# Performance work log

Hardware: AMD Instinct MI355X
Metric: run time of the kernel (lower is better)

Reference implementation:

```python
import jax, jax.numpy as jnp
import numpy as np
import math

N, D, F = 8192, 512, 2048
M, K = 4096, 128  # masked cells, masked genes per cell
EPS = 1e-5


def setup_inputs() -> dict:
    key = jax.random.key(0)
    ks = jax.random.split(key, 16)
    s = 0.02
    x = jax.random.normal(ks[0], (N, D), jnp.float32)
    # distinct masked cell indices (torch.randperm semantics)
    mask_nodes = jax.random.permutation(ks[1], N)[:M].astype(jnp.int64)
    # per-row distinct gene indices (torch.randperm per row)
    gene_idx = jnp.argsort(jax.random.uniform(ks[2], (M, D)), axis=1)[:, :K].astype(jnp.int64)
    return {
        'x': x, 'mask_nodes': mask_nodes, 'gene_idx': gene_idx,
        'Wq_e': s * jax.random.normal(ks[3], (D, D), jnp.float32),
        'Wk_e': s * jax.random.normal(ks[4], (D, D), jnp.float32),
        'Wv_e': s * jax.random.normal(ks[5], (D, D), jnp.float32),
        'ln1_g': jnp.ones((D,), jnp.float32), 'ln1_b': jnp.zeros((D,), jnp.float32),
        'ff_W1': s * jax.random.normal(ks[6], (D, F), jnp.float32),
        'ff_b1': jnp.zeros((F,), jnp.float32),
        'ff_W2': s * jax.random.normal(ks[7], (F, D), jnp.float32),
        'ff_b2': jnp.zeros((D,), jnp.float32),
        'ln2_g': jnp.ones((D,), jnp.float32), 'ln2_b': jnp.zeros((D,), jnp.float32),
        'Wq_d': s * jax.random.normal(ks[8], (D, D), jnp.float32),
        'Wk_d': s * jax.random.normal(ks[9], (D, D), jnp.float32),
        'Wv_d': s * jax.random.normal(ks[10], (D, D), jnp.float32),
        'ln3_g': jnp.ones((D,), jnp.float32), 'ln3_b': jnp.zeros((D,), jnp.float32),
        'ln4_g': jnp.ones((D,), jnp.float32), 'ln4_b': jnp.zeros((D,), jnp.float32),
        'head_W': s * jax.random.normal(ks[11], (D, D), jnp.float32),
        'head_b': jnp.zeros((D,), jnp.float32),
    }


def _ln(h, g, b):
    mu = jnp.mean(h, axis=-1, keepdims=True)
    var = jnp.mean(jnp.square(h - mu), axis=-1, keepdims=True)
    return (h - mu) * jax.lax.rsqrt(var + EPS) * g + b


def _attn(h, Wq, Wk, Wv):
    Q = h @ Wq
    Kt = h @ Wk
    V = h @ Wv
    scores = (Q @ Kt.T) / math.sqrt(D)  # [N, N]
    attn = jax.nn.softmax(scores, axis=-1)
    return attn @ V, attn


def _ff(h, W1, b1, W2, b2):
    return jax.nn.gelu(h @ W1 + b1, approximate=False) @ W2 + b2


def reference(x, mask_nodes, gene_idx,
              Wq_e, Wk_e, Wv_e, ln1_g, ln1_b,
              ff_W1, ff_b1, ff_W2, ff_b2, ln2_g, ln2_b,
              Wq_d, Wk_d, Wv_d, ln3_g, ln3_b, ln4_g, ln4_b,
              head_W, head_b):
    # mask selected genes of selected cells to 0 (encoding_mask_nodes)
    rows = mask_nodes[:, None]
    use_x = x.at[rows, gene_idx].set(0.0)

    hidden, encode_weights = _attn(use_x, Wq_e, Wk_e, Wv_e)
    hidden = _ln(hidden + use_x, ln1_g, ln1_b)
    hidden = _ln(hidden + _ff(hidden, ff_W1, ff_b1, ff_W2, ff_b2), ln2_g, ln2_b)
    # NOTE: `hidden[mask_nodes][gene_mask] = 0` in the original torch code
    # writes into a copy produced by advanced indexing -> it is a no-op.

    recon, _ = _attn(hidden, Wq_d, Wk_d, Wv_d)
    recon = _ln(recon + hidden, ln3_g, ln3_b)
    # original reuses self.ff (not self.ff1) in the decoder block
    recon = _ln(recon + _ff(recon, ff_W1, ff_b1, ff_W2, ff_b2), ln4_g, ln4_b)
    h = recon @ head_W + head_b

    x_init = x[rows, gene_idx]      # [M, K]
    x_recon = h[rows, gene_idx]     # [M, K]
    return (x_init, x_recon, encode_weights, recon)
```

## Files before the change

kernel.cpp:

```cpp
#include <hip/hip_runtime.h>
#include <hip/hip_bf16.h>
#include <stdint.h>
#include <math.h>

typedef __bf16 bf16_t;
typedef __bf16 bf16x8 __attribute__((ext_vector_type(8)));
typedef __bf16 bf16x4 __attribute__((ext_vector_type(4)));
typedef float floatx4 __attribute__((ext_vector_type(4)));

#define NN 8192
#define DD 512
#define FF 2048
#define MM 4096
#define KK 128

template<typename T> struct V16;
template<> struct V16<bf16_t> { using t = bf16x8;  static const int sh = 3; };
template<> struct V16<float>  { using t = floatx4; static const int sh = 2; };

__device__ __forceinline__ void async_copy16(const void* g, void* l) {
    __builtin_amdgcn_global_load_lds(
        (const __attribute__((address_space(1))) void*)(uintptr_t)g,
        (__attribute__((address_space(3))) void*)(uint32_t)(uintptr_t)l,
        16, 0, 0);
}

template<int EPI, typename OT>
__global__ __launch_bounds__(256)
void gemm_nt(const bf16_t* __restrict__ A, const bf16_t* __restrict__ B,
             OT* __restrict__ C,
             int M, int Nc, int Kd, int ldA, int ldB, int ldC,
             long partStride, float scale, const float* __restrict__ bias,
             float* __restrict__ denom)
{
    __shared__ char smem[16384];
    bf16_t* As = (bf16_t*)smem;
    bf16_t* Bs = (bf16_t*)(smem + 8192);

    const int tid  = threadIdx.x;
    const int lane = tid & 63;
    const int wave = tid >> 6;
    const int wm   = (wave >> 1) << 6;
    const int wn   = (wave & 1) << 6;
    const int quad = lane >> 4;
    const int l16  = lane & 15;

    const int gx   = gridDim.x;
    const int nwg  = gx * gridDim.y;
    const int orig = blockIdx.y * gx + blockIdx.x;
    const int swz  = (orig & 7) * (nwg >> 3) + (orig >> 3);
    const long bm  = (long)(swz % gx) * 128;
    const long bn  = (long)(swz / gx) * 128;

    const int  kchunk = Kd / gridDim.z;
    const long kBeg   = (long)blockIdx.z * kchunk;
    OT* __restrict__ Co = C + (long)blockIdx.z * partStride;

    const int t0 = tid, t1 = tid + 256;
    const bf16_t* pA0 = A + (bm + (t0 >> 2)) * (long)ldA + (t0 & 3) * 8 + kBeg;
    const bf16_t* pA1 = A + (bm + (t1 >> 2)) * (long)ldA + (t1 & 3) * 8 + kBeg;
    const bf16_t* pB0 = B + (bn + (t0 >> 2)) * (long)ldB + (t0 & 3) * 8 + kBeg;
    const bf16_t* pB1 = B + (bn + (t1 >> 2)) * (long)ldB + (t1 & 3) * 8 + kBeg;
    bf16_t* lA0 = &As[t0 * 8];
    bf16_t* lA1 = &As[t1 * 8];
    bf16_t* lB0 = &Bs[t0 * 8];
    bf16_t* lB1 = &Bs[t1 * 8];

    floatx4 acc[4][4] = {};

    for (long k0 = 0; k0 < kchunk; k0 += 32) {
        async_copy16(pA0 + k0, lA0);
        async_copy16(pA1 + k0, lA1);
        async_copy16(pB0 + k0, lB0);
        async_copy16(pB1 + k0, lB1);
        __syncthreads();

        bf16x8 af[4], bfr[4];
#pragma unroll
        for (int i = 0; i < 4; i++) {
            af[i]  = *(const bf16x8*)&As[(wm + i * 16 + l16) * 32 + quad * 8];
            bfr[i] = *(const bf16x8*)&Bs[(wn + i * 16 + l16) * 32 + quad * 8];
        }
#pragma unroll
        for (int mi = 0; mi < 4; mi++)
#pragma unroll
            for (int ni = 0; ni < 4; ni++)
                acc[mi][ni] = __builtin_amdgcn_mfma_f32_16x16x32_bf16(
                    af[mi], bfr[ni], acc[mi][ni], 0, 0, 0);
        __syncthreads();
    }

    OT* sm = (OT*)smem;
    const int g = wm >> 6;
#pragma unroll
    for (int mi = 0; mi < 4; mi++) {
        if (mi) __syncthreads();
        const long rbase = bm + wm + mi * 16 + quad * 4;
        if (EPI == 4) {
#pragma unroll
            for (int r = 0; r < 4; r++) {
                float rsum = 0.0f;
#pragma unroll
                for (int ni = 0; ni < 4; ni++) {
                    float v = __expf(acc[mi][ni][r] * scale);
                    rsum += v;
                    sm[(g * 16 + quad * 4 + r) * 128 + wn + ni * 16 + l16] = (OT)v;
                }
                rsum += __shfl_xor(rsum, 1);
                rsum += __shfl_xor(rsum, 2);
                rsum += __shfl_xor(rsum, 4);
                rsum += __shfl_xor(rsum, 8);
                if (l16 == 0) atomicAdd(denom + rbase + r, rsum);
            }
        } else {
#pragma unroll
            for (int ni = 0; ni < 4; ni++) {
                float bv = (EPI >= 2) ? bias[bn + wn + ni * 16 + l16] : 0.0f;
#pragma unroll
                for (int r = 0; r < 4; r++) {
                    float v = acc[mi][ni][r];
                    if (EPI == 1) v *= scale;
                    if (EPI >= 2) v += bv;
                    if (EPI == 3) v = 0.5f * v * (1.0f + erff(v * 0.70710678118f));
                    sm[(g * 16 + quad * 4 + r) * 128 + wn + ni * 16 + l16] = (OT)v;
                }
            }
        }
        __syncthreads();
        typedef typename V16<OT>::t VT;
        const int VSH = V16<OT>::sh;
        const int VEC = 1 << VSH;
        const int NP  = (32 * 128) / (256 * VEC);
#pragma unroll
        for (int p = 0; p < NP; p++) {
            const int vid  = p * 256 + tid;
            const int lrow = vid >> (7 - VSH);
            const int vcol = vid & ((128 >> VSH) - 1);
            const long grow = bm + (lrow >> 4) * 64 + mi * 16 + (lrow & 15);
            *(VT*)&Co[grow * (long)ldC + bn + vcol * VEC] =
                *(const VT*)&sm[lrow * 128 + vcol * VEC];
        }
    }
}

template<int EPI, typename OT>
static void launch_gemm(const bf16_t* A, const bf16_t* B, OT* C,
                        int M, int Nc, int Kd, int lda, int ldb, int ldc,
                        int splitk, long partStride, float scale,
                        const float* bias, float* denom, hipStream_t s)
{
    dim3 g(M / 128, Nc / 128, splitk);
    gemm_nt<EPI, OT><<<g, 256, 0, s>>>(A, B, C, M, Nc, Kd, lda, ldb, ldc,
                                       partStride, scale, bias, denom);
}

__global__ __launch_bounds__(256)
void transpose_f2b(const float* __restrict__ in, bf16_t* __restrict__ out,
                   int R, int C)
{
    __shared__ float tile[32][33];
    const int bx = blockIdx.x * 32;
    const int by = blockIdx.y * 32;
    const int tx = threadIdx.x, ty = threadIdx.y;
#pragma unroll
    for (int i = 0; i < 32; i += 8)
        tile[ty + i][tx] = in[(long)(by + ty + i) * C + bx + tx];
    __syncthreads();
#pragma unroll
    for (int i = 0; i < 32; i += 8)
        out[(long)(bx + ty + i) * R + by + tx] = (bf16_t)tile[tx][ty + i];
}

__global__ __launch_bounds__(256)
void transpose_b2b(const bf16_t* __restrict__ in, bf16_t* __restrict__ out,
                   int R, int C, int ldin)
{
    __shared__ bf16_t tile[32][34];
    const int bx = blockIdx.x * 32;
    const int by = blockIdx.y * 32;
    const int tx = threadIdx.x, ty = threadIdx.y;
#pragma unroll
    for (int i = 0; i < 32; i += 8)
        tile[ty + i][tx] = in[(long)(by + ty + i) * ldin + bx + tx];
    __syncthreads();
#pragma unroll
    for (int i = 0; i < 32; i += 8)
        out[(long)(bx + ty + i) * R + by + tx] = tile[tx][ty + i];
}

__global__ __launch_bounds__(256)
void encw_norm(const bf16_t* __restrict__ P, const float* __restrict__ denom,
               float* __restrict__ out)
{
    const long row = blockIdx.x;
    const float inv = 1.0f / denom[row];
    const bf16_t* p = P + row * (long)NN;
    float* q = out + row * (long)NN;
    const int tid = threadIdx.x;
#pragma unroll
    for (int i = 0; i < 4; i++) {
        const int o = (tid + i * 256) * 8;
        bf16x8 v = *(const bf16x8*)(p + o);
        float4 lo, hi;
        lo.x = (float)v[0] * inv; lo.y = (float)v[1] * inv;
        lo.z = (float)v[2] * inv; lo.w = (float)v[3] * inv;
        hi.x = (float)v[4] * inv; hi.y = (float)v[5] * inv;
        hi.z = (float)v[6] * inv; hi.w = (float)v[7] * inv;
        *(float4*)(q + o)     = lo;
        *(float4*)(q + o + 4) = hi;
    }
}

__global__ __launch_bounds__(256)
void zero_f32(float* __restrict__ p)
{
    p[blockIdx.x * 256 + threadIdx.x] = 0.0f;
}

template<int NP, bool RS, bool CB>
__global__ __launch_bounds__(64)
void add_ln_gen(const float* __restrict__ a, long pstride,
                const float* __restrict__ rs, const float* __restrict__ cb,
                const float* __restrict__ b,
                const float* __restrict__ g, const float* __restrict__ be,
                bf16_t* __restrict__ ob, float* __restrict__ of)
{
    const long row = blockIdx.x;
    const int lane = threadIdx.x;
    const long base = row * DD + lane * 8;
    const float irs = RS ? (1.0f / rs[row]) : 1.0f;
    float v[8], s = 0.0f, s2 = 0.0f;
#pragma unroll
    for (int j = 0; j < 8; j++) {
        float t = 0.0f;
#pragma unroll
        for (int p = 0; p < NP; p++) t += a[base + j + p * pstride];
        t *= irs;
        if (CB) t += cb[lane * 8 + j];
        t += b[base + j];
        v[j] = t;
        s += t; s2 += t * t;
    }
#pragma unroll
    for (int off = 32; off > 0; off >>= 1) {
        s  += __shfl_xor(s,  off);
        s2 += __shfl_xor(s2, off);
    }
    const float mu  = s * (1.0f / DD);
    const float var = s2 * (1.0f / DD) - mu * mu;
    const float inv = rsqrtf(var + 1e-5f);
    bf16x8 o;
#pragma unroll
    for (int j = 0; j < 8; j++) {
        float r = (v[j] - mu) * inv * g[lane * 8 + j] + be[lane * 8 + j];
        o[j] = (bf16_t)r;
        of[base + j] = r;
    }
    *(bf16x8*)(ob + base) = o;
}

__global__ __launch_bounds__(256)
void build_usex(const float* __restrict__ x, bf16_t* __restrict__ ub,
                float* __restrict__ uf)
{
    const long i = ((long)blockIdx.x * 256 + threadIdx.x) * 4;
    const float4 v = *(const float4*)(x + i);
    *(float4*)(uf + i) = v;
    bf16x4 o = { (bf16_t)v.x, (bf16_t)v.y, (bf16_t)v.z, (bf16_t)v.w };
    *(bf16x4*)(ub + i) = o;
}

__global__ __launch_bounds__(256)
void scatter_zero(bf16_t* __restrict__ ub, float* __restrict__ uf,
                  const int* __restrict__ mn, const int* __restrict__ gi)
{
    const int i = blockIdx.x * 256 + threadIdx.x;
    const long idx = (long)mn[i >> 7] * DD + gi[i];
    ub[idx] = (bf16_t)0.0f;
    uf[idx] = 0.0f;
}

__global__ __launch_bounds__(256)
void gather_mk(const float* __restrict__ src, const int* __restrict__ mn,
               const int* __restrict__ gi, float* __restrict__ dst)
{
    const int i = blockIdx.x * 256 + threadIdx.x;
    dst[i] = src[(long)mn[i >> 7] * DD + gi[i]];
}

__global__ __launch_bounds__(256)
void gather_head(const float* __restrict__ p1, long pstride,
                 const float* __restrict__ hb, const int* __restrict__ mn,
                 const int* __restrict__ gi, float* __restrict__ dst)
{
    const int i = blockIdx.x * 256 + threadIdx.x;
    const int col = gi[i];
    const long idx = (long)mn[i >> 7] * DD + col;
    dst[i] = p1[idx] + p1[idx + pstride] + hb[col];
}

extern "C" void kernel_launch(void* const* d_in, const int* in_sizes, int n_in,
                              void* d_out, int out_size, void* d_ws, size_t ws_size,
                              hipStream_t stream)
{
    const float* x      = (const float*)d_in[0];
    const int*   mn     = (const int*)d_in[1];
    const int*   gi     = (const int*)d_in[2];
    const float* Wq_e   = (const float*)d_in[3];
    const float* Wk_e   = (const float*)d_in[4];
    const float* Wv_e   = (const float*)d_in[5];
    const float* ln1_g  = (const float*)d_in[6];
    const float* ln1_b  = (const float*)d_in[7];
    const float* ff_W1  = (const float*)d_in[8];
    const float* ff_b1  = (const float*)d_in[9];
    const float* ff_W2  = (const float*)d_in[10];
    const float* ff_b2  = (const float*)d_in[11];
    const float* ln2_g  = (const float*)d_in[12];
    const float* ln2_b  = (const float*)d_in[13];
    const float* Wq_d   = (const float*)d_in[14];
    const float* Wk_d   = (const float*)d_in[15];
    const float* Wv_d   = (const float*)d_in[16];
    const float* ln3_g  = (const float*)d_in[17];
    const float* ln3_b  = (const float*)d_in[18];
    const float* ln4_g  = (const float*)d_in[19];
    const float* ln4_b  = (const float*)d_in[20];
    const float* head_W = (const float*)d_in[21];
    const float* head_b = (const float*)d_in[22];

    float* outf     = (float*)d_out;
    float* o_xinit  = outf;
    float* o_xrecon = outf + (size_t)MM * KK;
    float* o_encw   = outf + (size_t)2 * MM * KK;
    float* o_recon  = o_encw + (size_t)NN * NN;

    char* ws = (char*)d_ws;
    size_t off = 0;
    auto alloc = [&](size_t bytes) -> void* {
        void* p = ws + off;
        off += (bytes + 255) & ~(size_t)255;
        return p;
    };
    const size_t NDb = (size_t)NN * DD * sizeof(bf16_t);
    const size_t NDf = (size_t)NN * DD * sizeof(float);
    const long   NDe = (long)NN * DD;

    bf16_t* usex_b = (bf16_t*)alloc(NDb);
    bf16_t* qkv_b  = (bf16_t*)alloc((size_t)NN * 3 * DD * 2);
    bf16_t* vt_b   = (bf16_t*)alloc(NDb);
    bf16_t* hid_b  = (bf16_t*)alloc(NDb);
    float*  usex_f = (float*)alloc(NDf);
    float*  resA_f = (float*)alloc(NDf);
    float*  part_f = (float*)alloc(4 * NDf);
    bf16_t* wt_qe  = (bf16_t*)alloc((size_t)DD * DD * 2);
    bf16_t* wt_ke  = (bf16_t*)alloc((size_t)DD * DD * 2);
    bf16_t* wt_ve  = (bf16_t*)alloc((size_t)DD * DD * 2);
    bf16_t* wt_qd  = (bf16_t*)alloc((size_t)DD * DD * 2);
    bf16_t* wt_kd  = (bf16_t*)alloc((size_t)DD * DD * 2);
    bf16_t* wt_vd  = (bf16_t*)alloc((size_t)DD * DD * 2);
    bf16_t* wt_h   = (bf16_t*)alloc((size_t)DD * DD * 2);
    bf16_t* w1t    = (bf16_t*)alloc((size_t)DD * FF * 2);
    bf16_t* w2t    = (bf16_t*)alloc((size_t)FF * DD * 2);
    float*  denom  = (float*)alloc((size_t)NN * sizeof(float));
    bf16_t* scores = (bf16_t*)alloc((size_t)NN * NN * 2);
    bf16_t* t1_b   = scores;
    float*  resB_f = usex_f;
    (void)ws_size; (void)in_sizes; (void)n_in; (void)out_size;
    (void)wt_ke; (void)wt_ve; (void)wt_kd; (void)wt_vd;

    auto tr = [&](const float* in, bf16_t* o, int R, int C) {
        transpose_f2b<<<dim3(C / 32, R / 32), dim3(32, 8), 0, stream>>>(in, o, R, C);
    };
    const float SC = 0.04419417382f;

    tr(Wq_e, wt_qe, DD, DD);  tr(Wk_e, wt_ke, DD, DD);  tr(Wv_e, wt_ve, DD, DD);
    tr(Wq_d, wt_qd, DD, DD);  tr(Wk_d, wt_kd, DD, DD);  tr(Wv_d, wt_vd, DD, DD);
    tr(head_W, wt_h, DD, DD); tr(ff_W1, w1t, DD, FF);   tr(ff_W2, w2t, FF, DD);

    build_usex<<<NN * DD / 1024, 256, 0, stream>>>(x, usex_b, usex_f);
    scatter_zero<<<MM * KK / 256, 256, 0, stream>>>(usex_b, usex_f, mn, gi);
    gather_mk<<<MM * KK / 256, 256, 0, stream>>>(x, mn, gi, o_xinit);

    launch_gemm<0, bf16_t>(usex_b, wt_qe, qkv_b,
                           NN, 3 * DD, DD, DD, DD, 3 * DD, 1, 0, 0.f, nullptr,
                           nullptr, stream);
    transpose_b2b<<<dim3(DD / 32, NN / 32), dim3(32, 8), 0, stream>>>(
        qkv_b + 2 * DD, vt_b, NN, DD, 3 * DD);
    zero_f32<<<NN / 256, 256, 0, stream>>>(denom);
    launch_gemm<4, bf16_t>(qkv_b, qkv_b + DD, scores,
                           NN, NN, DD, 3 * DD, 3 * DD, NN, 1, 0, SC, nullptr,
                           denom, stream);
    encw_norm<<<NN, 256, 0, stream>>>(scores, denom, o_encw);
    launch_gemm<0, float>(scores, vt_b, part_f,
                          NN, DD, NN, NN, NN, DD, 4, NDe, 0.f, nullptr,
                          nullptr, stream);
    add_ln_gen<4, true, false><<<NN, 64, 0, stream>>>(
        part_f, NDe, denom, nullptr, usex_f, ln1_g, ln1_b, hid_b, resA_f);

    launch_gemm<3, bf16_t>(hid_b, w1t, t1_b,
                           NN, FF, DD, DD, DD, FF, 1, 0, 0.f, ff_b1,
                           nullptr, stream);
    launch_gemm<0, float>(t1_b, w2t, part_f,
                          NN, DD, FF, FF, FF, DD, 4, NDe, 0.f, nullptr,
                          nullptr, stream);
    add_ln_gen<4, false, true><<<NN, 64, 0, stream>>>(
        part_f, NDe, nullptr, ff_b2, resA_f, ln2_g, ln2_b, hid_b, resB_f);

    launch_gemm<0, bf16_t>(hid_b, wt_qd, qkv_b,
                           NN, 3 * DD, DD, DD, DD, 3 * DD, 1, 0, 0.f, nullptr,
                           nullptr, stream);
    transpose_b2b<<<dim3(DD / 32, NN / 32), dim3(32, 8), 0, stream>>>(
        qkv_b + 2 * DD, vt_b, NN, DD, 3 * DD);
    zero_f32<<<NN / 256, 256, 0, stream>>>(denom);
    launch_gemm<4, bf16_t>(qkv_b, qkv_b + DD, scores,
                           NN, NN, DD, 3 * DD, 3 * DD, NN, 1, 0, SC, nullptr,
                           denom, stream);
    launch_gemm<0, float>(scores, vt_b, part_f,
                          NN, DD, NN, NN, NN, DD, 4, NDe, 0.f, nullptr,
                          nullptr, stream);
    add_ln_gen<4, true, false><<<NN, 64, 0, stream>>>(
        part_f, NDe, denom, nullptr, resB_f, ln3_g, ln3_b, hid_b, resA_f);

    launch_gemm<3, bf16_t>(hid_b, w1t, t1_b,
                           NN, FF, DD, DD, DD, FF, 1, 0, 0.f, ff_b1,
                           nullptr, stream);
    launch_gemm<0, float>(t1_b, w2t, part_f,
                          NN, DD, FF, FF, FF, DD, 4, NDe, 0.f, nullptr,
                          nullptr, stream);
    add_ln_gen<4, false, true><<<NN, 64, 0, stream>>>(
        part_f, NDe, nullptr, ff_b2, resA_f, ln4_g, ln4_b, hid_b, o_recon);

    launch_gemm<0, float>(hid_b, wt_h, part_f,
                          NN, DD, DD, DD, DD, DD, 2, NDe, 0.f, nullptr,
                          nullptr, stream);
    gather_head<<<MM * KK / 256, 256, 0, stream>>>(part_f, NDe, head_b,
                                                   mn, gi, o_xrecon);
}
```

Measured before the change: 1.266 ms.

## Double-buffer GEMM LDS tiles and halve split-K partitions

The GEMM main loop now uses two LDS buffers, issuing the async global-to-LDS copy for the next K tile while MFMAs run on the current one. This hides load latency and removes one barrier per tile. LDS doubles to 32 KB and launch bounds request 3 blocks per CU. Split-K for the NxD GEMMs drops from 4 to 2, which halves the partial-sum buffer traffic read by the add+LN kernels but gives fewer blocks per GEMM.

```diff
diff --git a/kernel.cpp b/kernel.cpp
--- a/kernel.cpp
+++ b/kernel.cpp
@@ -26,16 +26,18 @@
 }
 
 template<int EPI, typename OT>
-__global__ __launch_bounds__(256)
+__global__ __launch_bounds__(256, 3)
 void gemm_nt(const bf16_t* __restrict__ A, const bf16_t* __restrict__ B,
              OT* __restrict__ C,
              int M, int Nc, int Kd, int ldA, int ldB, int ldC,
              long partStride, float scale, const float* __restrict__ bias,
              float* __restrict__ denom)
 {
-    __shared__ char smem[16384];
-    bf16_t* As = (bf16_t*)smem;
-    bf16_t* Bs = (bf16_t*)(smem + 8192);
+    __shared__ char smem[32768];
+    bf16_t* As0 = (bf16_t*)smem;
+    bf16_t* As1 = As0 + 4096;
+    bf16_t* Bs0 = As0 + 8192;
+    bf16_t* Bs1 = As0 + 12288;
 
     const int tid  = threadIdx.x;
     const int lane = tid & 63;
@@ -61,25 +63,21 @@
     const bf16_t* pA1 = A + (bm + (t1 >> 2)) * (long)ldA + (t1 & 3) * 8 + kBeg;
     const bf16_t* pB0 = B + (bn + (t0 >> 2)) * (long)ldB + (t0 & 3) * 8 + kBeg;
     const bf16_t* pB1 = B + (bn + (t1 >> 2)) * (long)ldB + (t1 & 3) * 8 + kBeg;
-    bf16_t* lA0 = &As[t0 * 8];
-    bf16_t* lA1 = &As[t1 * 8];
-    bf16_t* lB0 = &Bs[t0 * 8];
-    bf16_t* lB1 = &Bs[t1 * 8];
 
     floatx4 acc[4][4] = {};
 
-    for (long k0 = 0; k0 < kchunk; k0 += 32) {
-        async_copy16(pA0 + k0, lA0);
-        async_copy16(pA1 + k0, lA1);
-        async_copy16(pB0 + k0, lB0);
-        async_copy16(pB1 + k0, lB1);
-        __syncthreads();
-
+    auto stage = [&](bf16_t* Ab, bf16_t* Bb, long k0) {
+        async_copy16(pA0 + k0, Ab + t0 * 8);
+        async_copy16(pA1 + k0, Ab + t1 * 8);
+        async_copy16(pB0 + k0, Bb + t0 * 8);
+        async_copy16(pB1 + k0, Bb + t1 * 8);
+    };
+    auto compute = [&](const bf16_t* Ab, const bf16_t* Bb) {
         bf16x8 af[4], bfr[4];
 #pragma unroll
         for (int i = 0; i < 4; i++) {
-            af[i]  = *(const bf16x8*)&As[(wm + i * 16 + l16) * 32 + quad * 8];
-            bfr[i] = *(const bf16x8*)&Bs[(wn + i * 16 + l16) * 32 + quad * 8];
+            af[i]  = *(const bf16x8*)&Ab[(wm + i * 16 + l16) * 32 + quad * 8];
+            bfr[i] = *(const bf16x8*)&Bb[(wn + i * 16 + l16) * 32 + quad * 8];
         }
 #pragma unroll
         for (int mi = 0; mi < 4; mi++)
@@ -87,6 +85,18 @@
             for (int ni = 0; ni < 4; ni++)
                 acc[mi][ni] = __builtin_amdgcn_mfma_f32_16x16x32_bf16(
                     af[mi], bfr[ni], acc[mi][ni], 0, 0, 0);
+    };
+
+    const int nt = kchunk >> 5;
+    stage(As0, Bs0, 0);
+    __syncthreads();
+    long kk = 32;
+    for (int t = 0; t < nt; t += 2) {
+        stage(As1, Bs1, kk); kk += 32;
+        compute(As0, Bs0);
+        __syncthreads();
+        if (t + 2 < nt) { stage(As0, Bs0, kk); kk += 32; }
+        compute(As1, Bs1);
         __syncthreads();
     }
 
@@ -350,7 +360,7 @@
     bf16_t* hid_b  = (bf16_t*)alloc(NDb);
     float*  usex_f = (float*)alloc(NDf);
     float*  resA_f = (float*)alloc(NDf);
-    float*  part_f = (float*)alloc(4 * NDf);
+    float*  part_f = (float*)alloc(2 * NDf);
     bf16_t* wt_qe  = (bf16_t*)alloc((size_t)DD * DD * 2);
     bf16_t* wt_ke  = (bf16_t*)alloc((size_t)DD * DD * 2);
     bf16_t* wt_ve  = (bf16_t*)alloc((size_t)DD * DD * 2);
@@ -391,18 +401,18 @@
                            denom, stream);
     encw_norm<<<NN, 256, 0, stream>>>(scores, denom, o_encw);
     launch_gemm<0, float>(scores, vt_b, part_f,
-                          NN, DD, NN, NN, NN, DD, 4, NDe, 0.f, nullptr,
+                          NN, DD, NN, NN, NN, DD, 2, NDe, 0.f, nullptr,
                           nullptr, stream);
-    add_ln_gen<4, true, false><<<NN, 64, 0, stream>>>(
+    add_ln_gen<2, true, false><<<NN, 64, 0, stream>>>(
         part_f, NDe, denom, nullptr, usex_f, ln1_g, ln1_b, hid_b, resA_f);
 
     launch_gemm<3, bf16_t>(hid_b, w1t, t1_b,
                            NN, FF, DD, DD, DD, FF, 1, 0, 0.f, ff_b1,
                            nullptr, stream);
     launch_gemm<0, float>(t1_b, w2t, part_f,
-                          NN, DD, FF, FF, FF, DD, 4, NDe, 0.f, nullptr,
+                          NN, DD, FF, FF, FF, DD, 2, NDe, 0.f, nullptr,
                           nullptr, stream);
-    add_ln_gen<4, false, true><<<NN, 64, 0, stream>>>(
+    add_ln_gen<2, false, true><<<NN, 64, 0, stream>>>(
         part_f, NDe, nullptr, ff_b2, resA_f, ln2_g, ln2_b, hid_b, resB_f);
 
     launch_gemm<0, bf16_t>(hid_b, wt_qd, qkv_b,
@@ -415,18 +425,18 @@
                            NN, NN, DD, 3 * DD, 3 * DD, NN, 1, 0, SC, nullptr,
                            denom, stream);
     launch_gemm<0, float>(scores, vt_b, part_f,
-                          NN, DD, NN, NN, NN, DD, 4, NDe, 0.f, nullptr,
+                          NN, DD, NN, NN, NN, DD, 2, NDe, 0.f, nullptr,
                           nullptr, stream);
-    add_ln_gen<4, true, false><<<NN, 64, 0, stream>>>(
+    add_ln_gen<2, true, false><<<NN, 64, 0, stream>>>(
         part_f, NDe, denom, nullptr, resB_f, ln3_g, ln3_b, hid_b, resA_f);
 
     launch_gemm<3, bf16_t>(hid_b, w1t, t1_b,
                            NN, FF, DD, DD, DD, FF, 1, 0, 0.f, ff_b1,
                            nullptr, stream);
     launch_gemm<0, float>(t1_b, w2t, part_f,
-                          NN, DD, FF, FF, FF, DD, 4, NDe, 0.f, nullptr,
+                          NN, DD, FF, FF, FF, DD, 2, NDe, 0.f, nullptr,
                           nullptr, stream);
-    add_ln_gen<4, false, true><<<NN, 64, 0, stream>>>(
+    add_ln_gen<2, false, true><<<NN, 64, 0, stream>>>(
         part_f, NDe, nullptr, ff_b2, resA_f, ln4_g, ln4_b, hid_b, o_recon);
 
     launch_gemm<0, float>(hid_b, wt_h, part_f,
```

Result: faster. 1.093 ms (-13.6%).
